# Kernel optimization log

Hardware: AMD Instinct MI355X
Metric: run time of the kernel (lower is better)

Reference implementation:

```python
import jax, jax.numpy as jnp
import numpy as np


def setup_inputs() -> dict:
    key = jax.random.key(0)
    ks = jax.random.split(key, 8)
    B, T, H, Hu = 128, 64, 1024, 512
    MJW = 64                    # max_jump_width
    J = 2 * MJW + 1             # size_jump_width_set_nn = 129
    N = 2 * T                   # HMM states (word states + null states)
    I = 64                      # source sentence length
    sc = 0.02
    return {
        "y_hidden": jax.random.normal(ks[0], (B, T, H), jnp.float32),
        # emission probs p(source word i | state s), strictly positive for log
        "emission": jax.random.uniform(ks[1], (B, N, I), jnp.float32, 1e-4, 1.0),
        "source_lengths": jax.random.randint(ks[2], (B,), 1, I + 1),
        "W1": jax.random.normal(ks[3], (H, Hu), jnp.float32) * sc,
        "b1": jnp.zeros((Hu,), jnp.float32),
        "W2": jax.random.normal(ks[4], (Hu, J), jnp.float32) * sc,
        "b2": jnp.zeros((J,), jnp.float32),
        "W3": jax.random.normal(ks[5], (Hu, 1), jnp.float32) * sc,
        "b3": jnp.zeros((1,), jnp.float32),
        "max_jump_width": MJW,
    }


def _build_transition(y_hidden, W1, b1, W2, b2, W3, b3, mjw):
    # Dense(tanh) -> Dense softmax jump-width distribution + Dense sigmoid p0
    B, T, _ = y_hidden.shape
    ts = jnp.tanh(y_hidden @ W1 + b1)                       # [B,T,Hu]
    jw = jax.nn.softmax(ts @ W2 + b2, axis=-1)              # [B,T,J]
    p0 = jax.nn.sigmoid(jnp.squeeze(ts @ W3 + b3, -1))      # [B,T]
    r = jnp.arange(T)
    # banded gather: transition[i, j] = jw[i, mjw + j - i]
    band_idx = mjw + r[None, :] - r[:, None]                # [T,T], in [0, J)
    band = jnp.take_along_axis(jw, band_idx[None], axis=2)  # [B,T,T]
    diag_p0 = jnp.eye(T, dtype=jw.dtype) * p0[:, :, None]   # [B,T,T]
    top = jnp.concatenate([band, diag_p0], axis=2)          # [B,T,2T]
    return jnp.concatenate([top, top], axis=1)              # [B,2T,2T]


def _forward_alignment(transition, emission, source_lengths):
    # Faithful translation of the tf.scan forward algorithm. tf.scan with no
    # initializer uses elems[0] as the initial accumulator and emits it as
    # output[0] (log part = ones, so the [0,0] element is 1.0).
    B, N, I = emission.shape
    em = jnp.transpose(emission, (2, 0, 1))                 # [I,B,N]
    alpha0 = jnp.broadcast_to(em[0][:, None, :], (B, N, N)) # rows all equal e_0
    L0 = jnp.ones((B,), emission.dtype)

    def step(carry, e):
        alpha, L = carry                                    # [B,N,N], [B]
        yi = e[:, None, :]                                  # rows of yi_prob identical
        m1 = jnp.matmul(alpha, transition)                  # [B,N,N]
        tmp = m1 * yi
        tmp = tmp / jnp.sum(tmp, axis=2, keepdims=True)     # row-normalized alpha
        m2 = jnp.matmul(transition, alpha) * yi             # [B,N,N]
        max_j = jnp.max(m2, axis=-1)[:, 0]                  # gather row 0 -> [B]
        state_prev = jnp.sum(m1, axis=1)                    # [B,N]
        state = jnp.log(e) + jnp.log(state_prev) - max_j[:, None]
        state_log = jnp.log(jnp.sum(jnp.exp(state), axis=-1))
        L_new = L + state_log + max_j                       # [B]
        return (tmp, L_new), L_new

    (_, _), logs = jax.lax.scan(step, (alpha0, L0), em[1:])  # [I-1,B]
    logs = jnp.concatenate([L0[None], logs], axis=0).T       # [B,I]
    idx = (source_lengths - 1)[:, None]
    return jnp.take_along_axis(logs, idx, axis=1)[:, 0]      # [B]


def reference(y_hidden, emission, source_lengths, W1, b1, W2, b2, W3, b3, max_jump_width):
    transition = _build_transition(y_hidden, W1, b1, W2, b2, W3, b3, max_jump_width)
    return _forward_alignment(transition, emission, source_lengths)
```

## Files before the change

kernel.cpp:

```cpp
#include <hip/hip_runtime.h>
#include <hip/hip_bf16.h>

typedef float f32x4 __attribute__((ext_vector_type(4)));
typedef __bf16 bf16x8 __attribute__((ext_vector_type(8)));
typedef unsigned short u16;

#define OFF_W1T  0u
#define OFF_W23B 1048576u
#define OFF_TS   1196032u

static __device__ __forceinline__ u16 f2bf(float x) {
    __bf16 h = (__bf16)x;
    return __builtin_bit_cast(u16, h);
}

__device__ __forceinline__ void gload16(const void* g, void* l) {
    __builtin_amdgcn_global_load_lds(
        (const __attribute__((address_space(1))) void*)g,
        (__attribute__((address_space(3))) void*)l,
        16, 0, 0);
}

__global__ __launch_bounds__(256) void prep_kernel(
    const float* __restrict__ W1, const float* __restrict__ W2,
    const float* __restrict__ W3,
    __bf16* __restrict__ W1T, __bf16* __restrict__ W23B)
{
    const int t = threadIdx.x;
    if (blockIdx.x < 128) {
        __shared__ __bf16 lds_t[64][72];
        const int kt = blockIdx.x >> 3, nt = blockIdx.x & 7;
        const int k0 = kt * 64, n0 = nt * 64;
        {
            const int kr = t >> 2, c0 = (t & 3) * 16;
            const float* src = W1 + (size_t)(k0 + kr) * 512 + n0 + c0;
            #pragma unroll
            for (int q = 0; q < 4; ++q) {
                float4 v = *(const float4*)(src + q * 4);
                lds_t[kr][c0 + q * 4 + 0] = (__bf16)v.x;
                lds_t[kr][c0 + q * 4 + 1] = (__bf16)v.y;
                lds_t[kr][c0 + q * 4 + 2] = (__bf16)v.z;
                lds_t[kr][c0 + q * 4 + 3] = (__bf16)v.w;
            }
        }
        __syncthreads();
        {
            const int nr = t >> 2, kc = (t & 3) * 16;
            bf16x8 o0, o1;
            #pragma unroll
            for (int j = 0; j < 8; ++j) o0[j] = lds_t[kc + j][nr];
            #pragma unroll
            for (int j = 0; j < 8; ++j) o1[j] = lds_t[kc + 8 + j][nr];
            __bf16* dst = W1T + (size_t)(n0 + nr) * 1024 + k0 + kc;
            *(bf16x8*)(dst)     = o0;
            *(bf16x8*)(dst + 8) = o1;
        }
    } else {
        int g = (blockIdx.x - 128) * 256 + t;
        if (g < 9216) {
            int n = g >> 6;
            int k8 = (g & 63) * 8;
            bf16x8 v;
            #pragma unroll
            for (int j = 0; j < 8; ++j) {
                int k = k8 + j;
                float x = 0.0f;
                if (n < 129) x = W2[(size_t)k * 129 + n];
                else if (n == 129) x = W3[k];
                v[j] = (__bf16)x;
            }
            int kk = k8 >> 5, lg = (k8 >> 3) & 3, ct = n >> 4, lr = n & 15;
            *(bf16x8*)&W23B[(((size_t)(kk * 9 + ct)) * 64 + lg * 16 + lr) * 8] = v;
        }
    }
}

__global__ __launch_bounds__(256, 2) void gemm1_kernel(
    const float* __restrict__ Y, const __bf16* __restrict__ W1T,
    const float* __restrict__ b1, u16* __restrict__ ts)
{
    __shared__ float  As[3][64 * 32];
    __shared__ __bf16 Bs[3][128 * 32];
    const int tid = threadIdx.x;
    const int m0 = blockIdx.x * 64, n0 = blockIdx.y * 128;
    const int wid = tid >> 6, lane = tid & 63;
    const int wr = wid >> 1, wc = wid & 1;
    const int lr = lane & 15, lg = lane >> 4;

    const int al = lane >> 3;
    const int au = (lane & 7) ^ al;
    const float* yA0 = Y + (size_t)(m0 + (wid * 2 + 0) * 8 + al) * 1024 + au * 4;
    const float* yA1 = Y + (size_t)(m0 + (wid * 2 + 1) * 8 + al) * 1024 + au * 4;
    const int bl = lane >> 2;
    const int bu = (lane & 3) ^ (bl & 3);
    const __bf16* wB0 = W1T + (size_t)(n0 + (wid * 2 + 0) * 16 + bl) * 1024 + bu * 8;
    const __bf16* wB1 = W1T + (size_t)(n0 + (wid * 2 + 1) * 16 + bl) * 1024 + bu * 8;

    f32x4 acc[2][4];
    #pragma unroll
    for (int m = 0; m < 2; m++)
        #pragma unroll
        for (int n = 0; n < 4; n++) { f32x4 z = {0.f,0.f,0.f,0.f}; acc[m][n] = z; }

#define STAGE(buf, kt) do { \
    gload16(yA0 + (kt) * 32, &As[buf][(wid * 2 + 0) * 256]); \
    gload16(yA1 + (kt) * 32, &As[buf][(wid * 2 + 1) * 256]); \
    gload16(wB0 + (kt) * 32, &Bs[buf][(wid * 2 + 0) * 512]); \
    gload16(wB1 + (kt) * 32, &Bs[buf][(wid * 2 + 1) * 512]); \
} while (0)

#define COMPUTE(buf) do { \
    bf16x8 af[2]; bf16x8 bfr[4]; \
    _Pragma("unroll") \
    for (int m = 0; m < 2; ++m) { \
        const int row = wr * 32 + m * 16 + lr; \
        const int r7 = row & 7; \
        float4 h0 = *(const float4*)&As[buf][row * 32 + (((lg * 2 + 0) ^ r7) * 4)]; \
        float4 h1 = *(const float4*)&As[buf][row * 32 + (((lg * 2 + 1) ^ r7) * 4)]; \
        bf16x8 tt; \
        tt[0]=(__bf16)h0.x; tt[1]=(__bf16)h0.y; tt[2]=(__bf16)h0.z; tt[3]=(__bf16)h0.w; \
        tt[4]=(__bf16)h1.x; tt[5]=(__bf16)h1.y; tt[6]=(__bf16)h1.z; tt[7]=(__bf16)h1.w; \
        af[m] = tt; \
    } \
    _Pragma("unroll") \
    for (int n = 0; n < 4; ++n) { \
        const int rowb = wc * 64 + n * 16 + lr; \
        bfr[n] = *(const bf16x8*)&Bs[buf][rowb * 32 + ((lg ^ (rowb & 3)) * 8)]; \
    } \
    __builtin_amdgcn_s_setprio(1); \
    _Pragma("unroll") \
    for (int m = 0; m < 2; ++m) \
        _Pragma("unroll") \
        for (int n = 0; n < 4; ++n) \
            acc[m][n] = __builtin_amdgcn_mfma_f32_16x16x32_bf16(af[m], bfr[n], acc[m][n], 0, 0, 0); \
    __builtin_amdgcn_s_setprio(0); \
} while (0)

#define KSTEP(buf, kt, VM, DO_STAGE) do { \
    asm volatile("s_waitcnt vmcnt(" #VM ")" ::: "memory"); \
    __builtin_amdgcn_s_barrier(); \
    COMPUTE(buf); \
    asm volatile("s_waitcnt lgkmcnt(0)" ::: "memory"); \
    __builtin_amdgcn_s_barrier(); \
    if (DO_STAGE) STAGE(buf, (kt) + 3); \
} while (0)

    STAGE(0, 0); STAGE(1, 1); STAGE(2, 2);
    #pragma unroll 1
    for (int base = 0; base < 27; base += 3) {
        KSTEP(0, base + 0, 8, 1);
        KSTEP(1, base + 1, 8, 1);
        KSTEP(2, base + 2, 8, 1);
    }
    KSTEP(0, 27, 8, 1);
    KSTEP(1, 28, 8, 1);
    KSTEP(2, 29, 8, 0);
    KSTEP(0, 30, 4, 0);
    KSTEP(1, 31, 0, 0);

    #pragma unroll
    for (int m = 0; m < 2; m++) {
        #pragma unroll
        for (int n = 0; n < 4; n++) {
            int col = n0 + wc * 64 + n * 16 + lr;
            float bias = b1[col];
            #pragma unroll
            for (int j = 0; j < 4; j++) {
                int row = m0 + wr * 32 + m * 16 + lg * 4 + j;
                float v = tanhf(acc[m][n][j] + bias);
                ts[(size_t)row * 512 + col] = f2bf(v);
            }
        }
    }
#undef STAGE
#undef COMPUTE
#undef KSTEP
}

__global__ __launch_bounds__(256, 1) void gemm2_recur_kernel(
    const u16* __restrict__ ts, const u16* __restrict__ W23B,
    const float* __restrict__ b2, const float* __restrict__ b3,
    const float* __restrict__ em, const int* __restrict__ slen,
    float* __restrict__ out)
{
    __shared__ float jwT_s[64][65];
    __shared__ float em_s[128][65];
    __shared__ float p0_s[64];
    __shared__ f32x4 a_bc4[16];
    const int b = blockIdx.x;
    const int tid = threadIdx.x;
    const int w = tid >> 6, lane = tid & 63;
    const int lr = lane & 15, lg = lane >> 4;
    const int r0 = b * 64 + w * 16;

    {
        const float4* eg = (const float4*)(em + (size_t)b * 8192);
        #pragma unroll
        for (int q = 0; q < 8; ++q) {
            int i4 = tid + q * 256;
            float4 v = eg[i4];
            int base = i4 * 4; int n = base >> 6; int ii = base & 63;
            em_s[n][ii] = v.x; em_s[n][ii + 1] = v.y; em_s[n][ii + 2] = v.z; em_s[n][ii + 3] = v.w;
        }
    }

    f32x4 acc[9];
    #pragma unroll
    for (int ct = 0; ct < 9; ct++) { f32x4 z = {0.f,0.f,0.f,0.f}; acc[ct] = z; }

    #pragma unroll 4
    for (int kk = 0; kk < 16; ++kk) {
        bf16x8 a = *(const bf16x8*)(ts + (size_t)(r0 + lr) * 512 + kk * 32 + lg * 8);
        #pragma unroll
        for (int ct = 0; ct < 9; ct++) {
            bf16x8 bv = *(const bf16x8*)(W23B + ((size_t)(kk * 9 + ct) * 64 + lane) * 8);
            acc[ct] = __builtin_amdgcn_mfma_f32_16x16x32_bf16(a, bv, acc[ct], 0, 0, 0);
        }
    }

    float b3v = b3[0];
    #pragma unroll
    for (int j = 0; j < 4; j++) {
        int rloc = w * 16 + lg * 4 + j;
        float v[9];
        float mx = -1e30f;
        #pragma unroll
        for (int ct = 0; ct < 9; ct++) {
            int col = ct * 16 + lr;
            if (col < 129) { float x = acc[ct][j] + b2[col]; v[ct] = x; mx = fmaxf(mx, x); }
            else v[ct] = -1e30f;
        }
        #pragma unroll
        for (int o = 1; o < 16; o <<= 1) mx = fmaxf(mx, __shfl_xor(mx, o));
        float sum = 0.f;
        #pragma unroll
        for (int ct = 0; ct < 9; ct++) {
            int col = ct * 16 + lr;
            if (col < 129) { float e = expf(v[ct] - mx); v[ct] = e; sum += e; }
        }
        #pragma unroll
        for (int o = 1; o < 16; o <<= 1) sum += __shfl_xor(sum, o);
        float inv = 1.0f / sum;
        #pragma unroll
        for (int ct = 0; ct < 9; ct++) {
            int col = ct * 16 + lr;
            int cc = col - 64 + rloc;
            if (col < 129 && cc >= 0 && cc < 64)
                jwT_s[cc][rloc] = v[ct] * inv;
        }
        if (lr == 1) {
            float pv = acc[8][j] + b3v;
            p0_s[rloc] = 1.0f / (1.0f + expf(-pv));
        }
    }
    __syncthreads();
    if (tid >= 64) return;

    const int c = tid;
    f32x4 B0  = *(const f32x4*)&jwT_s[c][0];
    f32x4 B1  = *(const f32x4*)&jwT_s[c][4];
    f32x4 B2  = *(const f32x4*)&jwT_s[c][8];
    f32x4 B3  = *(const f32x4*)&jwT_s[c][12];
    f32x4 B4  = *(const f32x4*)&jwT_s[c][16];
    f32x4 B5  = *(const f32x4*)&jwT_s[c][20];
    f32x4 B6  = *(const f32x4*)&jwT_s[c][24];
    f32x4 B7  = *(const f32x4*)&jwT_s[c][28];
    f32x4 B8  = *(const f32x4*)&jwT_s[c][32];
    f32x4 B9  = *(const f32x4*)&jwT_s[c][36];
    f32x4 B10 = *(const f32x4*)&jwT_s[c][40];
    f32x4 B11 = *(const f32x4*)&jwT_s[c][44];
    f32x4 B12 = *(const f32x4*)&jwT_s[c][48];
    f32x4 B13 = *(const f32x4*)&jwT_s[c][52];
    f32x4 B14 = *(const f32x4*)&jwT_s[c][56];
    f32x4 B15 = *(const f32x4*)&jwT_s[c][60];
    const float p0r = p0_s[c];
    const int idx = slen[b] - 1;

    unsigned rbase = (unsigned)(uintptr_t)(__attribute__((address_space(3))) void*)&a_bc4[0];
    unsigned waddr = rbase + (unsigned)c * 4u;

    float ut = em_s[c][0] + em_s[c + 64][0];
    float Lacc = 0.f;

    #pragma unroll 1
    for (int i = 1; i <= idx; ++i) {
        float aloc = ut;
        f32x4 A0,A1,A2,A3,A4,A5,A6,A7,A8,A9,A10,A11,A12,A13,A14,A15;
        asm volatile(
            "ds_write_b32 %17, %16\n\t"
            "s_waitcnt lgkmcnt(0)\n\t"
            "ds_read_b128 %0, %18 offset:0\n\t"
            "ds_read_b128 %1, %18 offset:16\n\t"
            "ds_read_b128 %2, %18 offset:32\n\t"
            "ds_read_b128 %3, %18 offset:48\n\t"
            "ds_read_b128 %4, %18 offset:64\n\t"
            "ds_read_b128 %5, %18 offset:80\n\t"
            "ds_read_b128 %6, %18 offset:96\n\t"
            "ds_read_b128 %7, %18 offset:112\n\t"
            "ds_read_b128 %8, %18 offset:128\n\t"
            "ds_read_b128 %9, %18 offset:144\n\t"
            "ds_read_b128 %10, %18 offset:160\n\t"
            "ds_read_b128 %11, %18 offset:176\n\t"
            "ds_read_b128 %12, %18 offset:192\n\t"
            "ds_read_b128 %13, %18 offset:208\n\t"
            "ds_read_b128 %14, %18 offset:224\n\t"
            "ds_read_b128 %15, %18 offset:240\n\t"
            "s_waitcnt lgkmcnt(0)"
            : "=&v"(A0), "=&v"(A1), "=&v"(A2),  "=&v"(A3),
              "=&v"(A4), "=&v"(A5), "=&v"(A6),  "=&v"(A7),
              "=&v"(A8), "=&v"(A9), "=&v"(A10), "=&v"(A11),
              "=&v"(A12),"=&v"(A13),"=&v"(A14), "=&v"(A15)
            : "v"(ut), "v"(waddr), "v"(rbase)
            : "memory");
        float s0 = 0.f, s1 = 0.f, s2 = 0.f, s3 = 0.f;
#define ACC4(AV, BV) do { \
        s0 = fmaf((AV)[0], (BV)[0], s0); \
        s1 = fmaf((AV)[1], (BV)[1], s1); \
        s2 = fmaf((AV)[2], (BV)[2], s2); \
        s3 = fmaf((AV)[3], (BV)[3], s3); \
} while (0)
        ACC4(A0, B0);   ACC4(A1, B1);   ACC4(A2, B2);   ACC4(A3, B3);
        ACC4(A4, B4);   ACC4(A5, B5);   ACC4(A6, B6);   ACC4(A7, B7);
        ACC4(A8, B8);   ACC4(A9, B9);   ACC4(A10, B10); ACC4(A11, B11);
        ACC4(A12, B12); ACC4(A13, B13); ACC4(A14, B14); ACC4(A15, B15);
#undef ACC4
        ut = ((s0 + s1) + (s2 + s3)) * em_s[c][i] + aloc * p0r * em_s[c + 64][i];
        if (((i & 3) == 0) || (i == idx)) {
            float r = ut;
            #pragma unroll
            for (int o = 1; o < 64; o <<= 1) r += __shfl_xor(r, o);
            Lacc += __log2f(r);
            ut *= __builtin_amdgcn_rcpf(r);
        }
    }
    if (c == 0) out[b] = 1.0f + 0.6931471805599453f * (Lacc + 7.0f * (float)idx);
}

extern "C" void kernel_launch(void* const* d_in, const int* in_sizes, int n_in,
                              void* d_out, int out_size, void* d_ws, size_t ws_size,
                              hipStream_t stream)
{
    const float* Y   = (const float*)d_in[0];
    const float* em  = (const float*)d_in[1];
    const int*   sl  = (const int*)d_in[2];
    const float* W1  = (const float*)d_in[3];
    const float* b1  = (const float*)d_in[4];
    const float* W2  = (const float*)d_in[5];
    const float* b2  = (const float*)d_in[6];
    const float* W3  = (const float*)d_in[7];
    const float* b3  = (const float*)d_in[8];
    float* out = (float*)d_out;
    char* ws = (char*)d_ws;

    __bf16* W1T  = (__bf16*)(ws + OFF_W1T);
    __bf16* W23B = (__bf16*)(ws + OFF_W23B);
    u16*    ts   = (u16*)(ws + OFF_TS);

    prep_kernel<<<164, 256, 0, stream>>>(W1, W2, W3, W1T, W23B);
    dim3 g1(128, 4);
    gemm1_kernel<<<g1, 256, 0, stream>>>(Y, W1T, b1, ts);
    gemm2_recur_kernel<<<128, 256, 0, stream>>>(ts, (const u16*)W23B, b2, b3, em, sl, out);
}
```

Baseline: 83.07 us.

## Split band/softmax from recurrence and renormalize via exponent bits each step

Splits the fused gemm2+recurrence kernel into a band kernel, which writes the transposed jump-width band and p0 to workspace, and a 64-thread recurrence kernel that reads them from global memory. The periodic wave-wide sum, log and reciprocal renormalization is replaced by a per-step power-of-two rescale taken from the exponent of lane 0's value, with a single reduction and log at the end. This takes the cross-lane shuffles off the serial loop and frees the recurrence block from the 256-thread shape. In exchange it adds a kernel launch and a global round trip for the band data, and the rescale depends on lane 0's value being nonzero.

```diff
diff --git a/kernel.cpp b/kernel.cpp
--- a/kernel.cpp
+++ b/kernel.cpp
@@ -8,6 +8,8 @@
 #define OFF_W1T  0u
 #define OFF_W23B 1048576u
 #define OFF_TS   1196032u
+#define OFF_JWT  9584640u
+#define OFF_P0   11681792u
 
 static __device__ __forceinline__ u16 f2bf(float x) {
     __bf16 h = (__bf16)x;
@@ -177,33 +179,17 @@
 #undef KSTEP
 }
 
-__global__ __launch_bounds__(256, 1) void gemm2_recur_kernel(
+__global__ __launch_bounds__(256) void band_kernel(
     const u16* __restrict__ ts, const u16* __restrict__ W23B,
     const float* __restrict__ b2, const float* __restrict__ b3,
-    const float* __restrict__ em, const int* __restrict__ slen,
-    float* __restrict__ out)
-{
-    __shared__ float jwT_s[64][65];
-    __shared__ float em_s[128][65];
-    __shared__ float p0_s[64];
-    __shared__ f32x4 a_bc4[16];
+    float* __restrict__ jwT, float* __restrict__ p0)
+{
     const int b = blockIdx.x;
     const int tid = threadIdx.x;
     const int w = tid >> 6, lane = tid & 63;
     const int lr = lane & 15, lg = lane >> 4;
     const int r0 = b * 64 + w * 16;
 
-    {
-        const float4* eg = (const float4*)(em + (size_t)b * 8192);
-        #pragma unroll
-        for (int q = 0; q < 8; ++q) {
-            int i4 = tid + q * 256;
-            float4 v = eg[i4];
-            int base = i4 * 4; int n = base >> 6; int ii = base & 63;
-            em_s[n][ii] = v.x; em_s[n][ii + 1] = v.y; em_s[n][ii + 2] = v.z; em_s[n][ii + 3] = v.w;
-        }
-    }
-
     f32x4 acc[9];
     #pragma unroll
     for (int ct = 0; ct < 9; ct++) { f32x4 z = {0.f,0.f,0.f,0.f}; acc[ct] = z; }
@@ -246,41 +232,61 @@
             int col = ct * 16 + lr;
             int cc = col - 64 + rloc;
             if (col < 129 && cc >= 0 && cc < 64)
-                jwT_s[cc][rloc] = v[ct] * inv;
+                jwT[((size_t)b * 64 + cc) * 64 + rloc] = v[ct] * inv;
         }
         if (lr == 1) {
             float pv = acc[8][j] + b3v;
-            p0_s[rloc] = 1.0f / (1.0f + expf(-pv));
-        }
-    }
+            p0[b * 64 + rloc] = 1.0f / (1.0f + expf(-pv));
+        }
+    }
+}
+
+__global__ __launch_bounds__(64, 1) void recur_kernel(
+    const float* __restrict__ jwT, const float* __restrict__ p0g,
+    const float* __restrict__ em, const int* __restrict__ slen,
+    float* __restrict__ out)
+{
+    __shared__ float em_s[128][65];
+    __shared__ f32x4 a_bc4[16];
+    const int b = blockIdx.x, c = threadIdx.x;
+
+    const float* bb = jwT + ((size_t)b * 64 + c) * 64;
+    f32x4 B0  = *(const f32x4*)(bb + 0);
+    f32x4 B1  = *(const f32x4*)(bb + 4);
+    f32x4 B2  = *(const f32x4*)(bb + 8);
+    f32x4 B3  = *(const f32x4*)(bb + 12);
+    f32x4 B4  = *(const f32x4*)(bb + 16);
+    f32x4 B5  = *(const f32x4*)(bb + 20);
+    f32x4 B6  = *(const f32x4*)(bb + 24);
+    f32x4 B7  = *(const f32x4*)(bb + 28);
+    f32x4 B8  = *(const f32x4*)(bb + 32);
+    f32x4 B9  = *(const f32x4*)(bb + 36);
+    f32x4 B10 = *(const f32x4*)(bb + 40);
+    f32x4 B11 = *(const f32x4*)(bb + 44);
+    f32x4 B12 = *(const f32x4*)(bb + 48);
+    f32x4 B13 = *(const f32x4*)(bb + 52);
+    f32x4 B14 = *(const f32x4*)(bb + 56);
+    f32x4 B15 = *(const f32x4*)(bb + 60);
+
+    {
+        const float4* eg = (const float4*)(em + (size_t)b * 8192);
+        #pragma unroll 8
+        for (int q = 0; q < 32; ++q) {
+            int i4 = c + q * 64;
+            float4 v = eg[i4];
+            int base = i4 * 4; int n = base >> 6; int ii = base & 63;
+            em_s[n][ii] = v.x; em_s[n][ii + 1] = v.y; em_s[n][ii + 2] = v.z; em_s[n][ii + 3] = v.w;
+        }
+    }
+    const float p0r = p0g[b * 64 + c];
+    const int idx = slen[b] - 1;
     __syncthreads();
-    if (tid >= 64) return;
-
-    const int c = tid;
-    f32x4 B0  = *(const f32x4*)&jwT_s[c][0];
-    f32x4 B1  = *(const f32x4*)&jwT_s[c][4];
-    f32x4 B2  = *(const f32x4*)&jwT_s[c][8];
-    f32x4 B3  = *(const f32x4*)&jwT_s[c][12];
-    f32x4 B4  = *(const f32x4*)&jwT_s[c][16];
-    f32x4 B5  = *(const f32x4*)&jwT_s[c][20];
-    f32x4 B6  = *(const f32x4*)&jwT_s[c][24];
-    f32x4 B7  = *(const f32x4*)&jwT_s[c][28];
-    f32x4 B8  = *(const f32x4*)&jwT_s[c][32];
-    f32x4 B9  = *(const f32x4*)&jwT_s[c][36];
-    f32x4 B10 = *(const f32x4*)&jwT_s[c][40];
-    f32x4 B11 = *(const f32x4*)&jwT_s[c][44];
-    f32x4 B12 = *(const f32x4*)&jwT_s[c][48];
-    f32x4 B13 = *(const f32x4*)&jwT_s[c][52];
-    f32x4 B14 = *(const f32x4*)&jwT_s[c][56];
-    f32x4 B15 = *(const f32x4*)&jwT_s[c][60];
-    const float p0r = p0_s[c];
-    const int idx = slen[b] - 1;
+
+    float ut = em_s[c][0] + em_s[c + 64][0];
+    int Eacc = 0;
 
     unsigned rbase = (unsigned)(uintptr_t)(__attribute__((address_space(3))) void*)&a_bc4[0];
     unsigned waddr = rbase + (unsigned)c * 4u;
-
-    float ut = em_s[c][0] + em_s[c + 64][0];
-    float Lacc = 0.f;
 
     #pragma unroll 1
     for (int i = 1; i <= idx; ++i) {
@@ -325,15 +331,20 @@
         ACC4(A12, B12); ACC4(A13, B13); ACC4(A14, B14); ACC4(A15, B15);
 #undef ACC4
         ut = ((s0 + s1) + (s2 + s3)) * em_s[c][i] + aloc * p0r * em_s[c + 64][i];
-        if (((i & 3) == 0) || (i == idx)) {
-            float r = ut;
-            #pragma unroll
-            for (int o = 1; o < 64; o <<= 1) r += __shfl_xor(r, o);
-            Lacc += __log2f(r);
-            ut *= __builtin_amdgcn_rcpf(r);
-        }
-    }
-    if (c == 0) out[b] = 1.0f + 0.6931471805599453f * (Lacc + 7.0f * (float)idx);
+        int bits = __builtin_amdgcn_readfirstlane(__float_as_int(ut));
+        int ef = (bits >> 23) & 255;
+        Eacc += ef - 127;
+        ut *= __int_as_float((254 - ef) << 23);
+    }
+    float r = ut;
+    #pragma unroll
+    for (int o = 1; o < 64; o <<= 1) r += __shfl_xor(r, o);
+    if (c == 0) {
+        float res = 1.0f;
+        if (idx > 0)
+            res = 1.0f + 0.6931471805599453f * ((float)Eacc + __log2f(r) + 7.0f * (float)idx);
+        out[b] = res;
+    }
 }
 
 extern "C" void kernel_launch(void* const* d_in, const int* in_sizes, int n_in,
@@ -355,9 +366,12 @@
     __bf16* W1T  = (__bf16*)(ws + OFF_W1T);
     __bf16* W23B = (__bf16*)(ws + OFF_W23B);
     u16*    ts   = (u16*)(ws + OFF_TS);
+    float*  jwT  = (float*)(ws + OFF_JWT);
+    float*  p0   = (float*)(ws + OFF_P0);
 
     prep_kernel<<<164, 256, 0, stream>>>(W1, W2, W3, W1T, W23B);
     dim3 g1(128, 4);
     gemm1_kernel<<<g1, 256, 0, stream>>>(Y, W1T, b1, ts);
-    gemm2_recur_kernel<<<128, 256, 0, stream>>>(ts, (const u16*)W23B, b2, b3, em, sl, out);
-}
+    band_kernel<<<128, 256, 0, stream>>>(ts, (const u16*)W23B, b2, b3, jwT, p0);
+    recur_kernel<<<128, 64, 0, stream>>>(jwT, p0, em, sl, out);
+}
```

Result: slower. 85.07 us (+2.4%).
